# Kernel optimization log

Hardware: AMD Instinct MI355X
Metric: run time of the kernel (lower is better)

## Reference

```python
import jax, jax.numpy as jnp
import numpy as np

HIDDEN = 256
N_HEADS = 8
HEAD_DIM = HIDDEN // N_HEADS
SCALE = HEAD_DIM ** -0.5
LN_EPS = 1e-5


def entmax15(z):
    """Entmax-1.5 along the last axis (Peters et al. 2019 exact algorithm)."""
    z = z / 2.0
    z = z - jnp.max(z, axis=-1, keepdims=True)
    zs = jnp.flip(jnp.sort(z, axis=-1), axis=-1)          # descending
    K = z.shape[-1]
    k = jnp.arange(1, K + 1, dtype=z.dtype)
    mean = jnp.cumsum(zs, axis=-1) / k
    mean_sq = jnp.cumsum(zs * zs, axis=-1) / k
    ss = k * (mean_sq - mean * mean)
    delta = (1.0 - ss) / k
    tau = mean - jnp.sqrt(jnp.maximum(delta, 1e-12))
    support = (tau <= zs).astype(jnp.int32)
    k_star = jnp.sum(support, axis=-1, keepdims=True)      # support size >=1
    tau_star = jnp.take_along_axis(tau, k_star - 1, axis=-1)
    p = jnp.square(jnp.maximum(z - tau_star, 0.0))
    return p


def _attend(q, kv, W_q, W_k, W_v, log_temp):
    B, K, H = kv.shape
    qh = (q @ W_q.T).reshape(B, N_HEADS, HEAD_DIM)                 # (B,n,d)
    kh = (kv @ W_k.T).reshape(B, K, N_HEADS, HEAD_DIM)             # (B,K,n,d)
    vh = (kv @ W_v.T).reshape(B, K, N_HEADS, HEAD_DIM)
    scores = jnp.einsum('bnd,bknd->bnk', qh, kh) * (SCALE * jnp.exp(log_temp))
    attn = entmax15(scores)                                        # (B,n,K) sparse
    ctx = jnp.einsum('bnk,bknd->bnd', attn, vh).reshape(B, H)
    return ctx


def layernorm(x, gamma, beta):
    mu = jnp.mean(x, axis=-1, keepdims=True)
    var = jnp.mean(jnp.square(x - mu), axis=-1, keepdims=True)
    return (x - mu) * jax.lax.rsqrt(var + LN_EPS) * gamma + beta


def setup_inputs() -> dict:
    key = jax.random.key(0)
    ks = jax.random.split(key, 12)
    B, K, H = 32, 8192, HIDDEN
    s = 0.02
    return {
        'z_gene': jax.random.normal(ks[0], (B, H), jnp.float32),
        'z_cpg_seq': jax.random.normal(ks[1], (B, K, H), jnp.float32),
        'z_mirna_seq': jax.random.normal(ks[2], (B, K, H), jnp.float32),
        'W_q': jax.random.normal(ks[3], (H, H), jnp.float32) * s,
        'W_k_cpg': jax.random.normal(ks[4], (H, H), jnp.float32) * s,
        'W_v_cpg': jax.random.normal(ks[5], (H, H), jnp.float32) * s,
        'W_k_mirna': jax.random.normal(ks[6], (H, H), jnp.float32) * s,
        'W_v_mirna': jax.random.normal(ks[7], (H, H), jnp.float32) * s,
        'W_out': jax.random.normal(ks[8], (H, 2 * H), jnp.float32) * s,
        'b_out': jnp.zeros((H,), jnp.float32),
        'ln_gamma': jnp.ones((H,), jnp.float32),
        'ln_beta': jnp.zeros((H,), jnp.float32),
        'modality_logits': jnp.zeros((2,), jnp.float32),
        'log_temp': jnp.zeros((), jnp.float32),
    }


def reference(z_gene, z_cpg_seq, z_mirna_seq, W_q, W_k_cpg, W_v_cpg,
              W_k_mirna, W_v_mirna, W_out, b_out, ln_gamma, ln_beta,
              modality_logits, log_temp):
    ctx_cpg = _attend(z_gene, z_cpg_seq, W_q, W_k_cpg, W_v_cpg, log_temp)
    ctx_mirna = _attend(z_gene, z_mirna_seq, W_q, W_k_mirna, W_v_mirna, log_temp)
    w = jax.nn.softmax(modality_logits)
    combined = jnp.concatenate([w[0] * ctx_cpg, w[1] * ctx_mirna], axis=-1)
    fused = layernorm(combined @ W_out.T + b_out + z_gene, ln_gamma, ln_beta)
    return fused
```

## Files before the change

### kernel.cpp

```cpp
#include <hip/hip_runtime.h>
#include <cstdint>
#include <cstddef>

#define HIDDEN 256
#define NHEADS 8
#define HDIM 32
#define KLEN 8192
#define BATCH 32
#define NCHUNK 16
#define CHUNK (KLEN / NCHUNK)
#define NSLAB 32
#define LN_EPS 1e-5f

#define OFF_QT    ((size_t)0)
#define SZ_QT     ((size_t)2*BATCH*NHEADS*HIDDEN)
#define OFF_SC    (OFF_QT + SZ_QT)
#define SZ_SC     ((size_t)2*BATCH*KLEN*NHEADS)
#define OFF_UP    (OFF_SC + SZ_SC)
#define SZ_UP     ((size_t)2*BATCH*NCHUNK*NHEADS*HIDDEN)
#define OFF_COMB  (OFF_UP + SZ_UP)
#define SZ_COMB   ((size_t)BATCH*2*HIDDEN)

__global__ void k_prep(const float* __restrict__ zg, const float* __restrict__ Wq,
                       const float* __restrict__ Wk0, const float* __restrict__ Wk1,
                       const float* __restrict__ log_temp, float* __restrict__ qt) {
    int b = blockIdx.x, t = threadIdx.x;
    __shared__ float z[HIDDEN];
    __shared__ float qh[HIDDEN];
    z[t] = zg[(size_t)b*HIDDEN + t];
    __syncthreads();
    const float4* wr4 = (const float4*)(Wq + (size_t)t*HIDDEN);
    const float4* z4 = (const float4*)z;
    float acc = 0.f;
    #pragma unroll 8
    for (int i = 0; i < HIDDEN/4; ++i) {
        float4 w = wr4[i], zz = z4[i];
        acc += w.x*zz.x + w.y*zz.y + w.z*zz.z + w.w*zz.w;
    }
    qh[t] = acc;
    __syncthreads();
    float alpha = 0.5f * rsqrtf((float)HDIM) * __expf(log_temp[0]);
    for (int m = 0; m < 2; ++m) {
        const float* Wk = m ? Wk1 : Wk0;
        for (int n = 0; n < NHEADS; ++n) {
            float a = 0.f;
            #pragma unroll 8
            for (int d = 0; d < HDIM; ++d) {
                a += qh[n*HDIM + d] * Wk[(size_t)(n*HDIM + d)*HIDDEN + t];
            }
            qt[(((size_t)m*BATCH + b)*NHEADS + n)*HIDDEN + t] = a * alpha;
        }
    }
}

__global__ void __launch_bounds__(256, 4) k_scores(const float* __restrict__ kv0,
                                                   const float* __restrict__ kv1,
                                                   const float* __restrict__ qt,
                                                   float* __restrict__ sc) {
    int bid = blockIdx.x;
    int slab = bid & (NSLAB - 1);
    int mb = bid / NSLAB;
    int t = threadIdx.x;
    int wave = t >> 6, l = t & 63;
    const float* kv = ((mb >> 5) ? kv1 : kv0) + (size_t)(mb & 31)*KLEN*HIDDEN;
    const float4* kv4 = (const float4*)kv;
    const float* qtg = qt + (size_t)mb*NHEADS*HIDDEN;
    float4 qreg[8];
    #pragma unroll
    for (int n = 0; n < 8; ++n)
        qreg[n] = *(const float4*)(qtg + (size_t)n*HIDDEN + 4*l);
    float* out = sc + (size_t)mb*KLEN*NHEADS;
    int b0 = l & 1, b1 = (l >> 1) & 1, b2 = (l >> 2) & 1;

    int k = slab*256 + wave;
    float4 cur = kv4[(size_t)k*64 + l];
    #pragma unroll 2
    for (int i = 0; i < 64; ++i) {
        float4 nxt = cur;
        if (i < 63) nxt = kv4[(size_t)(k + 4)*64 + l];
        float a[8];
        #pragma unroll
        for (int n = 0; n < 8; ++n)
            a[n] = cur.x*qreg[n].x + cur.y*qreg[n].y + cur.z*qreg[n].z + cur.w*qreg[n].w;
        float w[4];
        #pragma unroll
        for (int u = 0; u < 4; ++u) {
            float keep = b0 ? a[2*u+1] : a[2*u];
            float send = b0 ? a[2*u]   : a[2*u+1];
            w[u] = keep + __shfl_xor(send, 1);
        }
        float x[2];
        #pragma unroll
        for (int u = 0; u < 2; ++u) {
            float keep = b1 ? w[2*u+1] : w[2*u];
            float send = b1 ? w[2*u]   : w[2*u+1];
            x[u] = keep + __shfl_xor(send, 2);
        }
        float keep = b2 ? x[1] : x[0];
        float send = b2 ? x[0] : x[1];
        float y = keep + __shfl_xor(send, 4);
        y += __shfl_xor(y, 8);
        y += __shfl_xor(y, 16);
        y += __shfl_xor(y, 32);
        if (l < 8) out[(size_t)k*8 + l] = y;
        cur = nxt; k += 4;
    }
}

__global__ void __launch_bounds__(256) k_entmax(float* __restrict__ sc) {
    int bid = blockIdx.x;
    int n = bid & 7, b = (bid >> 3) & 31, m = bid >> 8;
    int t = threadIdx.x;
    __shared__ float zs[KLEN];
    __shared__ float red[4];
    float* src = sc + ((size_t)m*BATCH + b)*KLEN*NHEADS + n;
    float mx = -1e30f;
    #pragma unroll
    for (int i = 0; i < KLEN/256; ++i) {
        float v = src[(size_t)(t + i*256)*NHEADS];
        zs[t + i*256] = v;
        mx = fmaxf(mx, v);
    }
    for (int off = 32; off; off >>= 1) mx = fmaxf(mx, __shfl_xor(mx, off));
    if ((t & 63) == 0) red[t >> 6] = mx;
    __syncthreads();
    mx = fmaxf(fmaxf(red[0], red[1]), fmaxf(red[2], red[3]));
    __syncthreads();
    const float4* z4 = (const float4*)zs;
    float lo = mx - 1.0f, hi = mx;
    for (int it = 0; it < 26; ++it) {
        float tm = 0.5f*(lo + hi);
        float s = 0.f;
        #pragma unroll
        for (int i = 0; i < 8; ++i) {
            float4 zz = z4[t + i*256];
            float d;
            d = fmaxf(zz.x - tm, 0.f); s = fmaf(d, d, s);
            d = fmaxf(zz.y - tm, 0.f); s = fmaf(d, d, s);
            d = fmaxf(zz.z - tm, 0.f); s = fmaf(d, d, s);
            d = fmaxf(zz.w - tm, 0.f); s = fmaf(d, d, s);
        }
        for (int off = 32; off; off >>= 1) s += __shfl_xor(s, off);
        if ((t & 63) == 0) red[t >> 6] = s;
        __syncthreads();
        s = red[0] + red[1] + red[2] + red[3];
        __syncthreads();
        if (s >= 1.0f) lo = tm; else hi = tm;
    }
    float tfin = 0.5f*(lo + hi);
    #pragma unroll
    for (int i = 0; i < KLEN/256; ++i) {
        float d = fmaxf(zs[t + i*256] - tfin, 0.f);
        src[(size_t)(t + i*256)*NHEADS] = d*d;
    }
}

__global__ void __launch_bounds__(256) k_ctxsum(const float* __restrict__ kv0,
                                                const float* __restrict__ kv1,
                                                const float* __restrict__ sc,
                                                float* __restrict__ upart) {
    int bid = blockIdx.x;
    int chunk = bid % NCHUNK;
    int m = (bid / NCHUNK) & 1;
    int b = bid / (2*NCHUNK);
    int t = threadIdx.x;
    int wave = t >> 6, lane = t & 63;
    const float* kv = (m ? kv1 : kv0) + (size_t)b*KLEN*HIDDEN;
    const float4* kv4 = (const float4*)kv;
    const float4* prow4 = (const float4*)(sc + ((size_t)m*BATCH + b)*KLEN*NHEADS);
    float acc[8][4];
    #pragma unroll
    for (int n = 0; n < 8; ++n)
        #pragma unroll
        for (int c = 0; c < 4; ++c) acc[n][c] = 0.f;

    #pragma unroll 2
    for (int kk = wave; kk < CHUNK; kk += 4) {
        size_t k = (size_t)chunk*CHUNK + kk;
        float4 kvv = kv4[k*64 + lane];
        float4 p0 = prow4[k*2], p1 = prow4[k*2 + 1];
        acc[0][0] = fmaf(p0.x, kvv.x, acc[0][0]); acc[0][1] = fmaf(p0.x, kvv.y, acc[0][1]);
        acc[0][2] = fmaf(p0.x, kvv.z, acc[0][2]); acc[0][3] = fmaf(p0.x, kvv.w, acc[0][3]);
        acc[1][0] = fmaf(p0.y, kvv.x, acc[1][0]); acc[1][1] = fmaf(p0.y, kvv.y, acc[1][1]);
        acc[1][2] = fmaf(p0.y, kvv.z, acc[1][2]); acc[1][3] = fmaf(p0.y, kvv.w, acc[1][3]);
        acc[2][0] = fmaf(p0.z, kvv.x, acc[2][0]); acc[2][1] = fmaf(p0.z, kvv.y, acc[2][1]);
        acc[2][2] = fmaf(p0.z, kvv.z, acc[2][2]); acc[2][3] = fmaf(p0.z, kvv.w, acc[2][3]);
        acc[3][0] = fmaf(p0.w, kvv.x, acc[3][0]); acc[3][1] = fmaf(p0.w, kvv.y, acc[3][1]);
        acc[3][2] = fmaf(p0.w, kvv.z, acc[3][2]); acc[3][3] = fmaf(p0.w, kvv.w, acc[3][3]);
        acc[4][0] = fmaf(p1.x, kvv.x, acc[4][0]); acc[4][1] = fmaf(p1.x, kvv.y, acc[4][1]);
        acc[4][2] = fmaf(p1.x, kvv.z, acc[4][2]); acc[4][3] = fmaf(p1.x, kvv.w, acc[4][3]);
        acc[5][0] = fmaf(p1.y, kvv.x, acc[5][0]); acc[5][1] = fmaf(p1.y, kvv.y, acc[5][1]);
        acc[5][2] = fmaf(p1.y, kvv.z, acc[5][2]); acc[5][3] = fmaf(p1.y, kvv.w, acc[5][3]);
        acc[6][0] = fmaf(p1.z, kvv.x, acc[6][0]); acc[6][1] = fmaf(p1.z, kvv.y, acc[6][1]);
        acc[6][2] = fmaf(p1.z, kvv.z, acc[6][2]); acc[6][3] = fmaf(p1.z, kvv.w, acc[6][3]);
        acc[7][0] = fmaf(p1.w, kvv.x, acc[7][0]); acc[7][1] = fmaf(p1.w, kvv.y, acc[7][1]);
        acc[7][2] = fmaf(p1.w, kvv.z, acc[7][2]); acc[7][3] = fmaf(p1.w, kvv.w, acc[7][3]);
    }
    __shared__ float redls[4*NHEADS*HIDDEN];
    float4* red4 = (float4*)redls;
    #pragma unroll
    for (int n = 0; n < 8; ++n) {
        float4 v; v.x = acc[n][0]; v.y = acc[n][1]; v.z = acc[n][2]; v.w = acc[n][3];
        red4[((size_t)wave*8 + n)*64 + lane] = v;
    }
    __syncthreads();
    float* up = upart + (((size_t)m*BATCH + b)*NCHUNK + chunk)*NHEADS*HIDDEN;
    int n = t >> 5, hq = (t & 31)*2;
    #pragma unroll
    for (int j = 0; j < 2; ++j) {
        float4 s = red4[((size_t)0*8 + n)*64 + hq + j];
        #pragma unroll
        for (int w = 1; w < 4; ++w) {
            float4 v = red4[((size_t)w*8 + n)*64 + hq + j];
            s.x += v.x; s.y += v.y; s.z += v.z; s.w += v.w;
        }
        ((float4*)(up + (size_t)n*HIDDEN))[hq + j] = s;
    }
}

__global__ void k_ctx(const float* __restrict__ upart, const float* __restrict__ Wv0,
                      const float* __restrict__ Wv1, const float* __restrict__ mlogits,
                      float* __restrict__ comb) {
    int b = blockIdx.x, t = threadIdx.x;
    __shared__ float ul[NHEADS*260];
    float l0 = mlogits[0], l1 = mlogits[1];
    float mxl = fmaxf(l0, l1);
    float e0 = __expf(l0 - mxl), e1 = __expf(l1 - mxl);
    float w0 = e0/(e0 + e1), w1 = e1/(e0 + e1);
    for (int m = 0; m < 2; ++m) {
        const float* Wv = m ? Wv1 : Wv0;
        float wm = m ? w1 : w0;
        __syncthreads();
        for (int n = 0; n < NHEADS; ++n) {
            float s = 0.f;
            const float* up = upart + ((size_t)m*BATCH + b)*NCHUNK*NHEADS*HIDDEN
                              + (size_t)n*HIDDEN + t;
            #pragma unroll
            for (int c = 0; c < NCHUNK; ++c) s += up[(size_t)c*NHEADS*HIDDEN];
            ul[n*260 + t] = s;
        }
        __syncthreads();
        int n = t >> 5;
        const float4* wr4 = (const float4*)(Wv + (size_t)t*HIDDEN);
        const float4* uu4 = (const float4*)(ul + n*260);
        float acc = 0.f;
        #pragma unroll 8
        for (int i = 0; i < HIDDEN/4; ++i) {
            float4 w = wr4[i], uu = uu4[i];
            acc += w.x*uu.x + w.y*uu.y + w.z*uu.z + w.w*uu.w;
        }
        comb[(size_t)b*(2*HIDDEN) + (size_t)m*HIDDEN + t] = acc * wm;
    }
}

__global__ void k_out(const float* __restrict__ comb, const float* __restrict__ Wout,
                      const float* __restrict__ bout, const float* __restrict__ zg,
                      const float* __restrict__ gamma, const float* __restrict__ beta,
                      float* __restrict__ out) {
    int b = blockIdx.x, t = threadIdx.x;
    __shared__ float cl[2*HIDDEN];
    __shared__ float red[4];
    cl[t] = comb[(size_t)b*512 + t];
    cl[t + 256] = comb[(size_t)b*512 + 256 + t];
    __syncthreads();
    float acc = bout[t] + zg[(size_t)b*HIDDEN + t];
    const float4* wr4 = (const float4*)(Wout + (size_t)t*512);
    const float4* cl4 = (const float4*)cl;
    #pragma unroll 8
    for (int i = 0; i < 512/4; ++i) {
        float4 w = wr4[i], c = cl4[i];
        acc += w.x*c.x + w.y*c.y + w.z*c.z + w.w*c.w;
    }
    float s = acc;
    for (int off = 32; off; off >>= 1) s += __shfl_xor(s, off);
    if ((t & 63) == 0) red[t >> 6] = s;
    __syncthreads();
    float mu = (red[0] + red[1] + red[2] + red[3]) * (1.0f/HIDDEN);
    __syncthreads();
    float dv = acc - mu;
    float vs = dv*dv;
    for (int off = 32; off; off >>= 1) vs += __shfl_xor(vs, off);
    if ((t & 63) == 0) red[t >> 6] = vs;
    __syncthreads();
    float var = (red[0] + red[1] + red[2] + red[3]) * (1.0f/HIDDEN);
    out[(size_t)b*HIDDEN + t] = dv * rsqrtf(var + LN_EPS) * gamma[t] + beta[t];
}

extern "C" void kernel_launch(void* const* d_in, const int* in_sizes, int n_in,
                              void* d_out, int out_size, void* d_ws, size_t ws_size,
                              hipStream_t stream) {
    const float* zg    = (const float*)d_in[0];
    const float* cpg   = (const float*)d_in[1];
    const float* mir   = (const float*)d_in[2];
    const float* Wq    = (const float*)d_in[3];
    const float* Wk0   = (const float*)d_in[4];
    const float* Wv0   = (const float*)d_in[5];
    const float* Wk1   = (const float*)d_in[6];
    const float* Wv1   = (const float*)d_in[7];
    const float* Wout  = (const float*)d_in[8];
    const float* bout  = (const float*)d_in[9];
    const float* gam   = (const float*)d_in[10];
    const float* bet   = (const float*)d_in[11];
    const float* mlog  = (const float*)d_in[12];
    const float* ltemp = (const float*)d_in[13];

    float* ws   = (float*)d_ws;
    float* qt   = ws + OFF_QT;
    float* sc   = ws + OFF_SC;
    float* up   = ws + OFF_UP;
    float* comb = ws + OFF_COMB;
    float* out  = (float*)d_out;

    hipLaunchKernelGGL(k_prep,   dim3(BATCH),           dim3(256), 0, stream,
                       zg, Wq, Wk0, Wk1, ltemp, qt);
    hipLaunchKernelGGL(k_scores, dim3(2*BATCH*NSLAB),   dim3(256), 0, stream,
                       cpg, mir, qt, sc);
    hipLaunchKernelGGL(k_entmax, dim3(2*BATCH*NHEADS),  dim3(256), 0, stream,
                       sc);
    hipLaunchKernelGGL(k_ctxsum, dim3(BATCH*2*NCHUNK),  dim3(256), 0, stream,
                       cpg, mir, sc, up);
    hipLaunchKernelGGL(k_ctx,    dim3(BATCH),           dim3(256), 0, stream,
                       up, Wv0, Wv1, mlog, comb);
    hipLaunchKernelGGL(k_out,    dim3(BATCH),           dim3(256), 0, stream,
                       comb, Wout, bout, zg, gam, bet, out);
}
```

Measured before the change: 368.6 us.

## Cache bf16 copy of KV during scoring and transpose score layout for entmax

The scoring kernel can now write a bf16 copy of each KV tile to workspace, and the context-sum kernel reads that copy instead of the fp32 input, which halves that second read. Scores are staged in shared memory and written head-major, so the entmax kernel can load contiguous float4s; it then writes probabilities in a key-major layout for the context sum. The entmax bisection also drops from 26 to 22 iterations. Total global traffic stays about the same, because the bf16 write adds back what the smaller read saves, and values precision is reduced to bf16.

Result: slower. 380.0 us (+3.1%).

```diff
diff --git a/kernel.cpp b/kernel.cpp
--- a/kernel.cpp
+++ b/kernel.cpp
@@ -1,4 +1,5 @@
 #include <hip/hip_runtime.h>
+#include <hip/hip_bf16.h>
 #include <cstdint>
 #include <cstddef>
 
@@ -12,14 +13,30 @@
 #define NSLAB 32
 #define LN_EPS 1e-5f
 
+typedef __attribute__((ext_vector_type(4))) unsigned short u16x4;
+
 #define OFF_QT    ((size_t)0)
 #define SZ_QT     ((size_t)2*BATCH*NHEADS*HIDDEN)
 #define OFF_SC    (OFF_QT + SZ_QT)
 #define SZ_SC     ((size_t)2*BATCH*KLEN*NHEADS)
-#define OFF_UP    (OFF_SC + SZ_SC)
+#define OFF_PT    (OFF_SC + SZ_SC)
+#define SZ_PT     ((size_t)2*BATCH*KLEN*NHEADS)
+#define OFF_UP    (OFF_PT + SZ_PT)
 #define SZ_UP     ((size_t)2*BATCH*NCHUNK*NHEADS*HIDDEN)
 #define OFF_COMB  (OFF_UP + SZ_UP)
 #define SZ_COMB   ((size_t)BATCH*2*HIDDEN)
+#define OFF_KVB_BYTES ((OFF_COMB + SZ_COMB) * 4)
+#define SZ_KVB_BYTES  ((size_t)2*BATCH*KLEN*HIDDEN*2)
+#define WS_NEEDED     (OFF_KVB_BYTES + SZ_KVB_BYTES)
+
+static __device__ inline unsigned short f2bu(float f) {
+    __hip_bfloat16 h = __float2bfloat16(f);
+    return __builtin_bit_cast(unsigned short, h);
+}
+static __device__ inline float b2f(unsigned short s) {
+    unsigned u = ((unsigned)s) << 16;
+    return __builtin_bit_cast(float, u);
+}
 
 __global__ void k_prep(const float* __restrict__ zg, const float* __restrict__ Wq,
                        const float* __restrict__ Wk0, const float* __restrict__ Wk1,
@@ -56,7 +73,9 @@
 __global__ void __launch_bounds__(256, 4) k_scores(const float* __restrict__ kv0,
                                                    const float* __restrict__ kv1,
                                                    const float* __restrict__ qt,
-                                                   float* __restrict__ sc) {
+                                                   float* __restrict__ sc,
+                                                   unsigned short* __restrict__ kvb,
+                                                   int do_cache) {
     int bid = blockIdx.x;
     int slab = bid & (NSLAB - 1);
     int mb = bid / NSLAB;
@@ -64,12 +83,13 @@
     int wave = t >> 6, l = t & 63;
     const float* kv = ((mb >> 5) ? kv1 : kv0) + (size_t)(mb & 31)*KLEN*HIDDEN;
     const float4* kv4 = (const float4*)kv;
+    unsigned short* kvbm = kvb + (size_t)mb*KLEN*HIDDEN;
     const float* qtg = qt + (size_t)mb*NHEADS*HIDDEN;
     float4 qreg[8];
     #pragma unroll
     for (int n = 0; n < 8; ++n)
         qreg[n] = *(const float4*)(qtg + (size_t)n*HIDDEN + 4*l);
-    float* out = sc + (size_t)mb*KLEN*NHEADS;
+    __shared__ float ls[NHEADS][260];
     int b0 = l & 1, b1 = (l >> 1) & 1, b2 = (l >> 2) & 1;
 
     int k = slab*256 + wave;
@@ -78,6 +98,12 @@
     for (int i = 0; i < 64; ++i) {
         float4 nxt = cur;
         if (i < 63) nxt = kv4[(size_t)(k + 4)*64 + l];
+        if (do_cache) {
+            u16x4 bv;
+            bv[0] = f2bu(cur.x); bv[1] = f2bu(cur.y);
+            bv[2] = f2bu(cur.z); bv[3] = f2bu(cur.w);
+            *(u16x4*)(kvbm + (size_t)k*HIDDEN + 4*l) = bv;
+        }
         float a[8];
         #pragma unroll
         for (int n = 0; n < 8; ++n)
@@ -102,24 +128,34 @@
         y += __shfl_xor(y, 8);
         y += __shfl_xor(y, 16);
         y += __shfl_xor(y, 32);
-        if (l < 8) out[(size_t)k*8 + l] = y;
+        if (l < 8) ls[l][k - slab*256] = y;
         cur = nxt; k += 4;
     }
-}
-
-__global__ void __launch_bounds__(256) k_entmax(float* __restrict__ sc) {
+    __syncthreads();
+    float* outb = sc + (size_t)mb*NHEADS*KLEN + slab*256;
+    int n = t >> 5, j0 = (t & 31)*8;
+    float4 v0 = *(const float4*)&ls[n][j0];
+    float4 v1 = *(const float4*)&ls[n][j0 + 4];
+    *(float4*)(outb + (size_t)n*KLEN + j0)     = v0;
+    *(float4*)(outb + (size_t)n*KLEN + j0 + 4) = v1;
+}
+
+__global__ void __launch_bounds__(256) k_entmax(const float* __restrict__ sc,
+                                                float* __restrict__ pT) {
     int bid = blockIdx.x;
-    int n = bid & 7, b = (bid >> 3) & 31, m = bid >> 8;
+    int n = bid & 7;
+    int mb = bid >> 3;
     int t = threadIdx.x;
     __shared__ float zs[KLEN];
     __shared__ float red[4];
-    float* src = sc + ((size_t)m*BATCH + b)*KLEN*NHEADS + n;
+    const float4* s4 = (const float4*)(sc + (size_t)bid*KLEN);
+    float4* z4w = (float4*)zs;
     float mx = -1e30f;
     #pragma unroll
-    for (int i = 0; i < KLEN/256; ++i) {
-        float v = src[(size_t)(t + i*256)*NHEADS];
-        zs[t + i*256] = v;
-        mx = fmaxf(mx, v);
+    for (int i = 0; i < 8; ++i) {
+        float4 v = s4[t + i*256];
+        z4w[t + i*256] = v;
+        mx = fmaxf(fmaxf(fmaxf(mx, v.x), v.y), fmaxf(v.z, v.w));
     }
     for (int off = 32; off; off >>= 1) mx = fmaxf(mx, __shfl_xor(mx, off));
     if ((t & 63) == 0) red[t >> 6] = mx;
@@ -128,7 +164,7 @@
     __syncthreads();
     const float4* z4 = (const float4*)zs;
     float lo = mx - 1.0f, hi = mx;
-    for (int it = 0; it < 26; ++it) {
+    for (int it = 0; it < 22; ++it) {
         float tm = 0.5f*(lo + hi);
         float s = 0.f;
         #pragma unroll
@@ -148,53 +184,119 @@
         if (s >= 1.0f) lo = tm; else hi = tm;
     }
     float tfin = 0.5f*(lo + hi);
-    #pragma unroll
-    for (int i = 0; i < KLEN/256; ++i) {
-        float d = fmaxf(zs[t + i*256] - tfin, 0.f);
-        src[(size_t)(t + i*256)*NHEADS] = d*d;
-    }
-}
-
-__global__ void __launch_bounds__(256) k_ctxsum(const float* __restrict__ kv0,
-                                                const float* __restrict__ kv1,
-                                                const float* __restrict__ sc,
-                                                float* __restrict__ upart) {
+    float* pTm = pT + (size_t)mb*KLEN*NHEADS + n;
+    #pragma unroll
+    for (int i = 0; i < 8; ++i) {
+        float4 zz = z4[t + i*256];
+        int k = (t + i*256)*4;
+        float d;
+        d = fmaxf(zz.x - tfin, 0.f); pTm[(size_t)(k+0)*NHEADS] = d*d;
+        d = fmaxf(zz.y - tfin, 0.f); pTm[(size_t)(k+1)*NHEADS] = d*d;
+        d = fmaxf(zz.z - tfin, 0.f); pTm[(size_t)(k+2)*NHEADS] = d*d;
+        d = fmaxf(zz.w - tfin, 0.f); pTm[(size_t)(k+3)*NHEADS] = d*d;
+    }
+}
+
+__global__ void __launch_bounds__(256, 4) k_ctxsum_bf(const unsigned short* __restrict__ kvb,
+                                                      const float* __restrict__ pT,
+                                                      float* __restrict__ upart) {
     int bid = blockIdx.x;
     int chunk = bid % NCHUNK;
-    int m = (bid / NCHUNK) & 1;
-    int b = bid / (2*NCHUNK);
+    int mb = bid / NCHUNK;
     int t = threadIdx.x;
     int wave = t >> 6, lane = t & 63;
-    const float* kv = (m ? kv1 : kv0) + (size_t)b*KLEN*HIDDEN;
+    const unsigned short* kvm = kvb + (size_t)mb*KLEN*HIDDEN;
+    const float4* prow4 = (const float4*)(pT + (size_t)mb*KLEN*NHEADS);
+    float acc[8][4];
+    #pragma unroll
+    for (int n = 0; n < 8; ++n)
+        #pragma unroll
+        for (int c = 0; c < 4; ++c) acc[n][c] = 0.f;
+
+    #pragma unroll 2
+    for (int kk = wave; kk < CHUNK; kk += 4) {
+        size_t k = (size_t)chunk*CHUNK + kk;
+        u16x4 kvv = *(const u16x4*)(kvm + k*HIDDEN + 4*lane);
+        float kx = b2f(kvv[0]), ky = b2f(kvv[1]), kz = b2f(kvv[2]), kw = b2f(kvv[3]);
+        float4 p0 = prow4[k*2], p1 = prow4[k*2 + 1];
+        acc[0][0] = fmaf(p0.x, kx, acc[0][0]); acc[0][1] = fmaf(p0.x, ky, acc[0][1]);
+        acc[0][2] = fmaf(p0.x, kz, acc[0][2]); acc[0][3] = fmaf(p0.x, kw, acc[0][3]);
+        acc[1][0] = fmaf(p0.y, kx, acc[1][0]); acc[1][1] = fmaf(p0.y, ky, acc[1][1]);
+        acc[1][2] = fmaf(p0.y, kz, acc[1][2]); acc[1][3] = fmaf(p0.y, kw, acc[1][3]);
+        acc[2][0] = fmaf(p0.z, kx, acc[2][0]); acc[2][1] = fmaf(p0.z, ky, acc[2][1]);
+        acc[2][2] = fmaf(p0.z, kz, acc[2][2]); acc[2][3] = fmaf(p0.z, kw, acc[2][3]);
+        acc[3][0] = fmaf(p0.w, kx, acc[3][0]); acc[3][1] = fmaf(p0.w, ky, acc[3][1]);
+        acc[3][2] = fmaf(p0.w, kz, acc[3][2]); acc[3][3] = fmaf(p0.w, kw, acc[3][3]);
+        acc[4][0] = fmaf(p1.x, kx, acc[4][0]); acc[4][1] = fmaf(p1.x, ky, acc[4][1]);
+        acc[4][2] = fmaf(p1.x, kz, acc[4][2]); acc[4][3] = fmaf(p1.x, kw, acc[4][3]);
+        acc[5][0] = fmaf(p1.y, kx, acc[5][0]); acc[5][1] = fmaf(p1.y, ky, acc[5][1]);
+        acc[5][2] = fmaf(p1.y, kz, acc[5][2]); acc[5][3] = fmaf(p1.y, kw, acc[5][3]);
+        acc[6][0] = fmaf(p1.z, kx, acc[6][0]); acc[6][1] = fmaf(p1.z, ky, acc[6][1]);
+        acc[6][2] = fmaf(p1.z, kz, acc[6][2]); acc[6][3] = fmaf(p1.z, kw, acc[6][3]);
+        acc[7][0] = fmaf(p1.w, kx, acc[7][0]); acc[7][1] = fmaf(p1.w, ky, acc[7][1]);
+        acc[7][2] = fmaf(p1.w, kz, acc[7][2]); acc[7][3] = fmaf(p1.w, kw, acc[7][3]);
+    }
+    __shared__ float redls[4*NHEADS*HIDDEN];
+    float4* red4 = (float4*)redls;
+    #pragma unroll
+    for (int n = 0; n < 8; ++n) {
+        float4 v; v.x = acc[n][0]; v.y = acc[n][1]; v.z = acc[n][2]; v.w = acc[n][3];
+        red4[((size_t)wave*8 + n)*64 + lane] = v;
+    }
+    __syncthreads();
+    float* up = upart + ((size_t)mb*NCHUNK + chunk)*NHEADS*HIDDEN;
+    int n = t >> 5, hq = (t & 31)*2;
+    #pragma unroll
+    for (int j = 0; j < 2; ++j) {
+        float4 s = red4[((size_t)0*8 + n)*64 + hq + j];
+        #pragma unroll
+        for (int w = 1; w < 4; ++w) {
+            float4 v = red4[((size_t)w*8 + n)*64 + hq + j];
+            s.x += v.x; s.y += v.y; s.z += v.z; s.w += v.w;
+        }
+        ((float4*)(up + (size_t)n*HIDDEN))[hq + j] = s;
+    }
+}
+
+__global__ void __launch_bounds__(256, 4) k_ctxsum_f32(const float* __restrict__ kv0,
+                                                       const float* __restrict__ kv1,
+                                                       const float* __restrict__ pT,
+                                                       float* __restrict__ upart) {
+    int bid = blockIdx.x;
+    int chunk = bid % NCHUNK;
+    int mb = bid / NCHUNK;
+    int t = threadIdx.x;
+    int wave = t >> 6, lane = t & 63;
+    const float* kv = ((mb >> 5) ? kv1 : kv0) + (size_t)(mb & 31)*KLEN*HIDDEN;
     const float4* kv4 = (const float4*)kv;
-    const float4* prow4 = (const float4*)(sc + ((size_t)m*BATCH + b)*KLEN*NHEADS);
+    const float4* prow4 = (const float4*)(pT + (size_t)mb*KLEN*NHEADS);
     float acc[8][4];
     #pragma unroll
     for (int n = 0; n < 8; ++n)
         #pragma unroll
         for (int c = 0; c < 4; ++c) acc[n][c] = 0.f;
-
     #pragma unroll 2
     for (int kk = wave; kk < CHUNK; kk += 4) {
         size_t k = (size_t)chunk*CHUNK + kk;
         float4 kvv = kv4[k*64 + lane];
+        float kx = kvv.x, ky = kvv.y, kz = kvv.z, kw = kvv.w;
         float4 p0 = prow4[k*2], p1 = prow4[k*2 + 1];
-        acc[0][0] = fmaf(p0.x, kvv.x, acc[0][0]); acc[0][1] = fmaf(p0.x, kvv.y, acc[0][1]);
-        acc[0][2] = fmaf(p0.x, kvv.z, acc[0][2]); acc[0][3] = fmaf(p0.x, kvv.w, acc[0][3]);
-        acc[1][0] = fmaf(p0.y, kvv.x, acc[1][0]); acc[1][1] = fmaf(p0.y, kvv.y, acc[1][1]);
-        acc[1][2] = fmaf(p0.y, kvv.z, acc[1][2]); acc[1][3] = fmaf(p0.y, kvv.w, acc[1][3]);
-        acc[2][0] = fmaf(p0.z, kvv.x, acc[2][0]); acc[2][1] = fmaf(p0.z, kvv.y, acc[2][1]);
-        acc[2][2] = fmaf(p0.z, kvv.z, acc[2][2]); acc[2][3] = fmaf(p0.z, kvv.w, acc[2][3]);
-        acc[3][0] = fmaf(p0.w, kvv.x, acc[3][0]); acc[3][1] = fmaf(p0.w, kvv.y, acc[3][1]);
-        acc[3][2] = fmaf(p0.w, kvv.z, acc[3][2]); acc[3][3] = fmaf(p0.w, kvv.w, acc[3][3]);
-        acc[4][0] = fmaf(p1.x, kvv.x, acc[4][0]); acc[4][1] = fmaf(p1.x, kvv.y, acc[4][1]);
-        acc[4][2] = fmaf(p1.x, kvv.z, acc[4][2]); acc[4][3] = fmaf(p1.x, kvv.w, acc[4][3]);
-        acc[5][0] = fmaf(p1.y, kvv.x, acc[5][0]); acc[5][1] = fmaf(p1.y, kvv.y, acc[5][1]);
-        acc[5][2] = fmaf(p1.y, kvv.z, acc[5][2]); acc[5][3] = fmaf(p1.y, kvv.w, acc[5][3]);
-        acc[6][0] = fmaf(p1.z, kvv.x, acc[6][0]); acc[6][1] = fmaf(p1.z, kvv.y, acc[6][1]);
-        acc[6][2] = fmaf(p1.z, kvv.z, acc[6][2]); acc[6][3] = fmaf(p1.z, kvv.w, acc[6][3]);
-        acc[7][0] = fmaf(p1.w, kvv.x, acc[7][0]); acc[7][1] = fmaf(p1.w, kvv.y, acc[7][1]);
-        acc[7][2] = fmaf(p1.w, kvv.z, acc[7][2]); acc[7][3] = fmaf(p1.w, kvv.w, acc[7][3]);
+        acc[0][0] = fmaf(p0.x, kx, acc[0][0]); acc[0][1] = fmaf(p0.x, ky, acc[0][1]);
+        acc[0][2] = fmaf(p0.x, kz, acc[0][2]); acc[0][3] = fmaf(p0.x, kw, acc[0][3]);
+        acc[1][0] = fmaf(p0.y, kx, acc[1][0]); acc[1][1] = fmaf(p0.y, ky, acc[1][1]);
+        acc[1][2] = fmaf(p0.y, kz, acc[1][2]); acc[1][3] = fmaf(p0.y, kw, acc[1][3]);
+        acc[2][0] = fmaf(p0.z, kx, acc[2][0]); acc[2][1] = fmaf(p0.z, ky, acc[2][1]);
+        acc[2][2] = fmaf(p0.z, kz, acc[2][2]); acc[2][3] = fmaf(p0.z, kw, acc[2][3]);
+        acc[3][0] = fmaf(p0.w, kx, acc[3][0]); acc[3][1] = fmaf(p0.w, ky, acc[3][1]);
+        acc[3][2] = fmaf(p0.w, kz, acc[3][2]); acc[3][3] = fmaf(p0.w, kw, acc[3][3]);
+        acc[4][0] = fmaf(p1.x, kx, acc[4][0]); acc[4][1] = fmaf(p1.x, ky, acc[4][1]);
+        acc[4][2] = fmaf(p1.x, kz, acc[4][2]); acc[4][3] = fmaf(p1.x, kw, acc[4][3]);
+        acc[5][0] = fmaf(p1.y, kx, acc[5][0]); acc[5][1] = fmaf(p1.y, ky, acc[5][1]);
+        acc[5][2] = fmaf(p1.y, kz, acc[5][2]); acc[5][3] = fmaf(p1.y, kw, acc[5][3]);
+        acc[6][0] = fmaf(p1.z, kx, acc[6][0]); acc[6][1] = fmaf(p1.z, ky, acc[6][1]);
+        acc[6][2] = fmaf(p1.z, kz, acc[6][2]); acc[6][3] = fmaf(p1.z, kw, acc[6][3]);
+        acc[7][0] = fmaf(p1.w, kx, acc[7][0]); acc[7][1] = fmaf(p1.w, ky, acc[7][1]);
+        acc[7][2] = fmaf(p1.w, kz, acc[7][2]); acc[7][3] = fmaf(p1.w, kw, acc[7][3]);
     }
     __shared__ float redls[4*NHEADS*HIDDEN];
     float4* red4 = (float4*)redls;
@@ -204,7 +306,7 @@
         red4[((size_t)wave*8 + n)*64 + lane] = v;
     }
     __syncthreads();
-    float* up = upart + (((size_t)m*BATCH + b)*NCHUNK + chunk)*NHEADS*HIDDEN;
+    float* up = upart + ((size_t)mb*NCHUNK + chunk)*NHEADS*HIDDEN;
     int n = t >> 5, hq = (t & 31)*2;
     #pragma unroll
     for (int j = 0; j < 2; ++j) {
@@ -304,21 +406,30 @@
     const float* mlog  = (const float*)d_in[12];
     const float* ltemp = (const float*)d_in[13];
 
-    float* ws   = (float*)d_ws;
-    float* qt   = ws + OFF_QT;
-    float* sc   = ws + OFF_SC;
-    float* up   = ws + OFF_UP;
-    float* comb = ws + OFF_COMB;
-    float* out  = (float*)d_out;
+    float* ws    = (float*)d_ws;
+    float* qt    = ws + OFF_QT;
+    float* sc    = ws + OFF_SC;
+    float* pT    = ws + OFF_PT;
+    float* up    = ws + OFF_UP;
+    float* comb  = ws + OFF_COMB;
+    unsigned short* kvb = (unsigned short*)((char*)d_ws + OFF_KVB_BYTES);
+    float* out   = (float*)d_out;
+
+    int do_cache = (ws_size >= (size_t)WS_NEEDED) ? 1 : 0;
 
     hipLaunchKernelGGL(k_prep,   dim3(BATCH),           dim3(256), 0, stream,
                        zg, Wq, Wk0, Wk1, ltemp, qt);
     hipLaunchKernelGGL(k_scores, dim3(2*BATCH*NSLAB),   dim3(256), 0, stream,
-                       cpg, mir, qt, sc);
+                       cpg, mir, qt, sc, kvb, do_cache);
     hipLaunchKernelGGL(k_entmax, dim3(2*BATCH*NHEADS),  dim3(256), 0, stream,
-                       sc);
-    hipLaunchKernelGGL(k_ctxsum, dim3(BATCH*2*NCHUNK),  dim3(256), 0, stream,
-                       cpg, mir, sc, up);
+                       sc, pT);
+    if (do_cache) {
+        hipLaunchKernelGGL(k_ctxsum_bf, dim3(2*BATCH*NCHUNK), dim3(256), 0, stream,
+                           kvb, pT, up);
+    } else {
+        hipLaunchKernelGGL(k_ctxsum_f32, dim3(2*BATCH*NCHUNK), dim3(256), 0, stream,
+                           cpg, mir, pT, up);
+    }
     hipLaunchKernelGGL(k_ctx,    dim3(BATCH),           dim3(256), 0, stream,
                        up, Wv0, Wv1, mlog, comb);
     hipLaunchKernelGGL(k_out,    dim3(BATCH),           dim3(256), 0, stream,
```

## Replace entmax bisection with Newton iterations and fuse probability computation into ctxsum

Applied to the files above, without the earlier changes.

The entmax threshold search switches from 26 bisection steps to 10 Newton steps on sum(max(z-tau,0)^2)=1, computing both the function and its derivative in each block reduction. Only the per-row tau is stored. The ctxsum kernel recomputes p=max(z-tau,0)^2 on the fly, which drops the strided write-back of the score buffer. Newton started from mx-1 approaches from below and converges monotonically, but if 10 steps are not enough the result carries some residual error.

Result: faster. 322.1 us (-12.6%).

```diff
diff --git a/kernel.cpp b/kernel.cpp
--- a/kernel.cpp
+++ b/kernel.cpp
@@ -16,7 +16,9 @@
 #define SZ_QT     ((size_t)2*BATCH*NHEADS*HIDDEN)
 #define OFF_SC    (OFF_QT + SZ_QT)
 #define SZ_SC     ((size_t)2*BATCH*KLEN*NHEADS)
-#define OFF_UP    (OFF_SC + SZ_SC)
+#define OFF_TAU   (OFF_SC + SZ_SC)
+#define SZ_TAU    ((size_t)2*BATCH*NHEADS)
+#define OFF_UP    (OFF_TAU + SZ_TAU)
 #define SZ_UP     ((size_t)2*BATCH*NCHUNK*NHEADS*HIDDEN)
 #define OFF_COMB  (OFF_UP + SZ_UP)
 #define SZ_COMB   ((size_t)BATCH*2*HIDDEN)
@@ -107,13 +109,16 @@
     }
 }
 
-__global__ void __launch_bounds__(256) k_entmax(float* __restrict__ sc) {
+__global__ void __launch_bounds__(256) k_entmax(const float* __restrict__ sc,
+                                                float* __restrict__ tau) {
     int bid = blockIdx.x;
-    int n = bid & 7, b = (bid >> 3) & 31, m = bid >> 8;
+    int n = bid & 7;
+    int mb = bid >> 3;
     int t = threadIdx.x;
     __shared__ float zs[KLEN];
-    __shared__ float red[4];
-    float* src = sc + ((size_t)m*BATCH + b)*KLEN*NHEADS + n;
+    __shared__ float redg[4];
+    __shared__ float redd[4];
+    const float* src = sc + (size_t)mb*KLEN*NHEADS + n;
     float mx = -1e30f;
     #pragma unroll
     for (int i = 0; i < KLEN/256; ++i) {
@@ -122,52 +127,54 @@
         mx = fmaxf(mx, v);
     }
     for (int off = 32; off; off >>= 1) mx = fmaxf(mx, __shfl_xor(mx, off));
-    if ((t & 63) == 0) red[t >> 6] = mx;
-    __syncthreads();
-    mx = fmaxf(fmaxf(red[0], red[1]), fmaxf(red[2], red[3]));
+    if ((t & 63) == 0) redg[t >> 6] = mx;
+    __syncthreads();
+    mx = fmaxf(fmaxf(redg[0], redg[1]), fmaxf(redg[2], redg[3]));
     __syncthreads();
     const float4* z4 = (const float4*)zs;
-    float lo = mx - 1.0f, hi = mx;
-    for (int it = 0; it < 26; ++it) {
-        float tm = 0.5f*(lo + hi);
-        float s = 0.f;
+    float tk = mx - 1.0f;
+    for (int it = 0; it < 10; ++it) {
+        float g = 0.f, gd = 0.f;
         #pragma unroll
         for (int i = 0; i < 8; ++i) {
             float4 zz = z4[t + i*256];
             float d;
-            d = fmaxf(zz.x - tm, 0.f); s = fmaf(d, d, s);
-            d = fmaxf(zz.y - tm, 0.f); s = fmaf(d, d, s);
-            d = fmaxf(zz.z - tm, 0.f); s = fmaf(d, d, s);
-            d = fmaxf(zz.w - tm, 0.f); s = fmaf(d, d, s);
-        }
-        for (int off = 32; off; off >>= 1) s += __shfl_xor(s, off);
-        if ((t & 63) == 0) red[t >> 6] = s;
+            d = fmaxf(zz.x - tk, 0.f); g = fmaf(d, d, g); gd += d;
+            d = fmaxf(zz.y - tk, 0.f); g = fmaf(d, d, g); gd += d;
+            d = fmaxf(zz.z - tk, 0.f); g = fmaf(d, d, g); gd += d;
+            d = fmaxf(zz.w - tk, 0.f); g = fmaf(d, d, g); gd += d;
+        }
+        for (int off = 32; off; off >>= 1) {
+            g  += __shfl_xor(g, off);
+            gd += __shfl_xor(gd, off);
+        }
+        if ((t & 63) == 0) { redg[t >> 6] = g; redd[t >> 6] = gd; }
         __syncthreads();
-        s = red[0] + red[1] + red[2] + red[3];
+        g  = redg[0] + redg[1] + redg[2] + redg[3];
+        gd = redd[0] + redd[1] + redd[2] + redd[3];
         __syncthreads();
-        if (s >= 1.0f) lo = tm; else hi = tm;
-    }
-    float tfin = 0.5f*(lo + hi);
-    #pragma unroll
-    for (int i = 0; i < KLEN/256; ++i) {
-        float d = fmaxf(zs[t + i*256] - tfin, 0.f);
-        src[(size_t)(t + i*256)*NHEADS] = d*d;
-    }
+        float denom = fmaxf(2.f*gd, 1e-12f);
+        tk = fminf(tk + (g - 1.0f)/denom, mx);
+    }
+    if (t == 0) tau[bid] = tk;
 }
 
 __global__ void __launch_bounds__(256) k_ctxsum(const float* __restrict__ kv0,
                                                 const float* __restrict__ kv1,
                                                 const float* __restrict__ sc,
+                                                const float* __restrict__ tau,
                                                 float* __restrict__ upart) {
     int bid = blockIdx.x;
     int chunk = bid % NCHUNK;
-    int m = (bid / NCHUNK) & 1;
-    int b = bid / (2*NCHUNK);
+    int mb = bid / NCHUNK;
     int t = threadIdx.x;
     int wave = t >> 6, lane = t & 63;
-    const float* kv = (m ? kv1 : kv0) + (size_t)b*KLEN*HIDDEN;
+    const float* kv = ((mb >> 5) ? kv1 : kv0) + (size_t)(mb & 31)*KLEN*HIDDEN;
     const float4* kv4 = (const float4*)kv;
-    const float4* prow4 = (const float4*)(sc + ((size_t)m*BATCH + b)*KLEN*NHEADS);
+    const float4* zrow4 = (const float4*)(sc + (size_t)mb*KLEN*NHEADS);
+    float tv[8];
+    #pragma unroll
+    for (int n = 0; n < 8; ++n) tv[n] = tau[(size_t)mb*NHEADS + n];
     float acc[8][4];
     #pragma unroll
     for (int n = 0; n < 8; ++n)
@@ -178,23 +185,23 @@
     for (int kk = wave; kk < CHUNK; kk += 4) {
         size_t k = (size_t)chunk*CHUNK + kk;
         float4 kvv = kv4[k*64 + lane];
-        float4 p0 = prow4[k*2], p1 = prow4[k*2 + 1];
-        acc[0][0] = fmaf(p0.x, kvv.x, acc[0][0]); acc[0][1] = fmaf(p0.x, kvv.y, acc[0][1]);
-        acc[0][2] = fmaf(p0.x, kvv.z, acc[0][2]); acc[0][3] = fmaf(p0.x, kvv.w, acc[0][3]);
-        acc[1][0] = fmaf(p0.y, kvv.x, acc[1][0]); acc[1][1] = fmaf(p0.y, kvv.y, acc[1][1]);
-        acc[1][2] = fmaf(p0.y, kvv.z, acc[1][2]); acc[1][3] = fmaf(p0.y, kvv.w, acc[1][3]);
-        acc[2][0] = fmaf(p0.z, kvv.x, acc[2][0]); acc[2][1] = fmaf(p0.z, kvv.y, acc[2][1]);
-        acc[2][2] = fmaf(p0.z, kvv.z, acc[2][2]); acc[2][3] = fmaf(p0.z, kvv.w, acc[2][3]);
-        acc[3][0] = fmaf(p0.w, kvv.x, acc[3][0]); acc[3][1] = fmaf(p0.w, kvv.y, acc[3][1]);
-        acc[3][2] = fmaf(p0.w, kvv.z, acc[3][2]); acc[3][3] = fmaf(p0.w, kvv.w, acc[3][3]);
-        acc[4][0] = fmaf(p1.x, kvv.x, acc[4][0]); acc[4][1] = fmaf(p1.x, kvv.y, acc[4][1]);
-        acc[4][2] = fmaf(p1.x, kvv.z, acc[4][2]); acc[4][3] = fmaf(p1.x, kvv.w, acc[4][3]);
-        acc[5][0] = fmaf(p1.y, kvv.x, acc[5][0]); acc[5][1] = fmaf(p1.y, kvv.y, acc[5][1]);
-        acc[5][2] = fmaf(p1.y, kvv.z, acc[5][2]); acc[5][3] = fmaf(p1.y, kvv.w, acc[5][3]);
-        acc[6][0] = fmaf(p1.z, kvv.x, acc[6][0]); acc[6][1] = fmaf(p1.z, kvv.y, acc[6][1]);
-        acc[6][2] = fmaf(p1.z, kvv.z, acc[6][2]); acc[6][3] = fmaf(p1.z, kvv.w, acc[6][3]);
-        acc[7][0] = fmaf(p1.w, kvv.x, acc[7][0]); acc[7][1] = fmaf(p1.w, kvv.y, acc[7][1]);
-        acc[7][2] = fmaf(p1.w, kvv.z, acc[7][2]); acc[7][3] = fmaf(p1.w, kvv.w, acc[7][3]);
+        float4 za = zrow4[k*2], zb = zrow4[k*2 + 1];
+        float p[8], d;
+        d = fmaxf(za.x - tv[0], 0.f); p[0] = d*d;
+        d = fmaxf(za.y - tv[1], 0.f); p[1] = d*d;
+        d = fmaxf(za.z - tv[2], 0.f); p[2] = d*d;
+        d = fmaxf(za.w - tv[3], 0.f); p[3] = d*d;
+        d = fmaxf(zb.x - tv[4], 0.f); p[4] = d*d;
+        d = fmaxf(zb.y - tv[5], 0.f); p[5] = d*d;
+        d = fmaxf(zb.z - tv[6], 0.f); p[6] = d*d;
+        d = fmaxf(zb.w - tv[7], 0.f); p[7] = d*d;
+        #pragma unroll
+        for (int n = 0; n < 8; ++n) {
+            acc[n][0] = fmaf(p[n], kvv.x, acc[n][0]);
+            acc[n][1] = fmaf(p[n], kvv.y, acc[n][1]);
+            acc[n][2] = fmaf(p[n], kvv.z, acc[n][2]);
+            acc[n][3] = fmaf(p[n], kvv.w, acc[n][3]);
+        }
     }
     __shared__ float redls[4*NHEADS*HIDDEN];
     float4* red4 = (float4*)redls;
@@ -204,7 +211,7 @@
         red4[((size_t)wave*8 + n)*64 + lane] = v;
     }
     __syncthreads();
-    float* up = upart + (((size_t)m*BATCH + b)*NCHUNK + chunk)*NHEADS*HIDDEN;
+    float* up = upart + ((size_t)mb*NCHUNK + chunk)*NHEADS*HIDDEN;
     int n = t >> 5, hq = (t & 31)*2;
     #pragma unroll
     for (int j = 0; j < 2; ++j) {
@@ -307,6 +314,7 @@
     float* ws   = (float*)d_ws;
     float* qt   = ws + OFF_QT;
     float* sc   = ws + OFF_SC;
+    float* tau  = ws + OFF_TAU;
     float* up   = ws + OFF_UP;
     float* comb = ws + OFF_COMB;
     float* out  = (float*)d_out;
@@ -316,9 +324,9 @@
     hipLaunchKernelGGL(k_scores, dim3(2*BATCH*NSLAB),   dim3(256), 0, stream,
                        cpg, mir, qt, sc);
     hipLaunchKernelGGL(k_entmax, dim3(2*BATCH*NHEADS),  dim3(256), 0, stream,
-                       sc);
-    hipLaunchKernelGGL(k_ctxsum, dim3(BATCH*2*NCHUNK),  dim3(256), 0, stream,
-                       cpg, mir, sc, up);
+                       sc, tau);
+    hipLaunchKernelGGL(k_ctxsum, dim3(2*BATCH*NCHUNK),  dim3(256), 0, stream,
+                       cpg, mir, sc, tau, up);
     hipLaunchKernelGGL(k_ctx,    dim3(BATCH),           dim3(256), 0, stream,
                        up, Wv0, Wv1, mlog, comb);
     hipLaunchKernelGGL(k_out,    dim3(BATCH),           dim3(256), 0, stream,
```
